# Optimization experiments

Measured on AMD Instinct MI355X. Metric: run time of the kernel, lower is better.

Reference implementation:

```python
import jax, jax.numpy as jnp
import numpy as np

WS, EXP, FW, HEADS = 7, 3, 7, 6
DIM = 192
HD = DIM // HEADS
SCALE = HD ** -0.5
POOL_K, POOL_PAD = 7, 3  # focal level k=0: kernel = 2*(FW//2) + 2**0 + (2**0 - 1) = 7, stride 1, pad 3
WA = WS * WS  # 49 tokens per window


def _rel_index():
    # identical formula for in-window bias and pooled-window bias (k_window = FW + 2**0 - 1 = 7 = WS)
    c = np.stack(np.meshgrid(np.arange(WS), np.arange(WS), indexing='ij')).reshape(2, -1)
    rel = (c[:, :, None] - c[:, None, :]).transpose(1, 2, 0).copy()
    rel[..., 0] += WS - 1
    rel[..., 1] += WS - 1
    rel[..., 0] *= 2 * WS - 1
    return rel.sum(-1)  # (49, 49) int indices into 169-entry tables


def _valid_rolled():
    m = np.ones((4, WS, WS), dtype=np.float32)
    m[0, :-EXP, :-EXP] = 0  # tl
    m[1, :-EXP, EXP:] = 0   # tr
    m[2, EXP:, :-EXP] = 0   # bl
    m[3, EXP:, EXP:] = 0    # br
    return np.nonzero(m.reshape(-1))[0]  # (132,)

REL_IDX = _rel_index()
VALID_ROLLED = _valid_rolled()


def _win_part(t):
    # (B,H,W,C) -> (B*nWin, WA, HEADS, HD)
    B, H, W, C = t.shape
    t = t.reshape(B, H // WS, WS, W // WS, WS, C).transpose(0, 1, 3, 2, 4, 5)
    return t.reshape(-1, WA, HEADS, HD)


def _unfold(t):
    # torch.nn.Unfold(kernel=7, stride=1, pad=3) on (B,h,w,C) -> (B*h*w, K*K, C)
    B, h, w, C = t.shape
    tp = jnp.pad(t, ((0, 0), (POOL_PAD, POOL_PAD), (POOL_PAD, POOL_PAD), (0, 0)))
    ii = np.arange(h)[:, None] + np.arange(POOL_K)[None, :]
    jj = np.arange(w)[:, None] + np.arange(POOL_K)[None, :]
    p = tp[:, ii][:, :, :, jj]            # (B, h, K, w, K, C)
    p = p.transpose(0, 1, 3, 2, 4, 5)     # (B, h, w, K, K, C)
    return p.reshape(B * h * w, POOL_K * POOL_K, C)


def setup_inputs() -> dict:
    key = jax.random.key(0)
    ks = jax.random.split(key, 9)
    B, H, W = 8, 112, 112
    nWh, nWw = H // WS, W // WS
    return {
        'x': jax.random.normal(ks[0], (B, H, W, DIM), jnp.float32),
        'x_pooled': jax.random.normal(ks[1], (B, nWh, nWw, DIM), jnp.float32),
        'qkv_w': jax.random.normal(ks[2], (3 * DIM, DIM), jnp.float32) * 0.02,
        'qkv_b': jax.random.normal(ks[3], (3 * DIM,), jnp.float32) * 0.02,
        'proj_w': jax.random.normal(ks[4], (DIM, DIM), jnp.float32) * 0.02,
        'proj_b': jax.random.normal(ks[5], (DIM,), jnp.float32) * 0.02,
        'rpb_table': jax.random.normal(ks[6], ((2 * WS - 1) ** 2, HEADS), jnp.float32) * 0.02,
        'rpb_neighbors': jax.random.normal(ks[7], (1, HEADS, WA, len(VALID_ROLLED)), jnp.float32) * 0.02,
        'rpb_windows': jax.random.normal(ks[8], (HEADS, (2 * WS - 1) ** 2), jnp.float32) * 0.02,
    }


def reference(x, x_pooled, qkv_w, qkv_b, proj_w, proj_b, rpb_table, rpb_neighbors, rpb_windows):
    B, H, W, C = x.shape
    # qkv on fine features
    qkv = x @ qkv_w.T + qkv_b                    # (B,H,W,3C)
    q, k, v = jnp.split(qkv, 3, axis=-1)
    qw = _win_part(q).transpose(0, 2, 1, 3)      # (BnW, heads, 49, hd)
    kw = _win_part(k).transpose(0, 2, 1, 3)
    vw = _win_part(v).transpose(0, 2, 1, 3)

    # rolled neighbor keys/values (tl, tr, bl, br), gather valid ring indices
    shifts = [(-EXP, -EXP), (-EXP, EXP), (EXP, -EXP), (EXP, EXP)]
    k_roll = jnp.concatenate([_win_part(jnp.roll(k, s, axis=(1, 2))) for s in shifts], axis=1)
    v_roll = jnp.concatenate([_win_part(jnp.roll(v, s, axis=(1, 2))) for s in shifts], axis=1)
    k_roll = k_roll.transpose(0, 2, 1, 3)[:, :, VALID_ROLLED]   # (BnW, heads, 132, hd)
    v_roll = v_roll.transpose(0, 2, 1, 3)[:, :, VALID_ROLLED]
    k_rolled = jnp.concatenate([kw, k_roll], axis=2)            # (BnW, heads, 181, hd)
    v_rolled = jnp.concatenate([vw, v_roll], axis=2)
    wa_rolled = k_rolled.shape[2]

    # focal level-0 pooled keys/values via unfold on the pooled map
    _, nWh, nWw, _ = x_pooled.shape
    qkv_p = x_pooled @ qkv_w.T + qkv_b
    _, kp, vp = jnp.split(qkv_p, 3, axis=-1)
    k_pool = _unfold(kp).reshape(-1, POOL_K * POOL_K, HEADS, HD).transpose(0, 2, 1, 3)  # (BnW, heads, 49, hd)
    v_pool = _unfold(vp).reshape(-1, POOL_K * POOL_K, HEADS, HD).transpose(0, 2, 1, 3)
    # validity mask from unfolding an all-ones map (zero padding -> -100)
    um = _unfold(jnp.ones((1, nWh, nWw, 1), x.dtype))[..., 0]   # (nWin, 49)
    pool_mask = jnp.where(um == 0, jnp.asarray(-100.0, x.dtype), jnp.asarray(0.0, x.dtype))

    k_all = jnp.concatenate([k_rolled, k_pool], axis=2)          # (BnW, heads, 230, hd)
    v_all = jnp.concatenate([v_rolled, v_pool], axis=2)

    attn = jnp.einsum('bhqd,bhkd->bhqk', qw * SCALE, k_all)      # (BnW, heads, 49, 230)

    # relative position biases, concatenated along the key axis
    bias_win = rpb_table[REL_IDX.reshape(-1)].reshape(WA, WA, HEADS).transpose(2, 0, 1)     # (heads,49,49)
    bias_pool = rpb_windows[:, REL_IDX.reshape(-1)].reshape(HEADS, WA, WA)                  # (heads,49,49)
    bias = jnp.concatenate([bias_win, rpb_neighbors[0], bias_pool], axis=-1)                # (heads,49,230)
    attn = attn + bias[None]
    # boundary mask on the pooled slice, tiled per batch
    mask_b = jnp.tile(pool_mask, (B, 1))[:, None, None, :]       # (BnW,1,1,49)
    attn = attn.at[..., wa_rolled:].add(mask_b)

    attn = jax.nn.softmax(attn, axis=-1)
    out = jnp.einsum('bhqk,bhkd->bqhd', attn, v_all).reshape(-1, WA, C)
    return out @ proj_w.T + proj_b                               # (B*nWin, 49, C)
```

## Files before the change

kernel.cpp:

```cpp
#include <hip/hip_runtime.h>
#include <stdint.h>


#define DIM 192
#define HEADS 6
#define HD 32
#define WA 49
#define NKEY 230
#define VSTR 264
#define SSTR2 136
#define SCALE_F 0.17677669529663687f
#define LOG2E 1.4426950408889634f
#define PM_NEG (-144.26950408889634f)
#define NFINE 100352
#define POOLBASE (NFINE * DIM)

typedef __attribute__((ext_vector_type(8))) short bf16x8;
typedef __attribute__((ext_vector_type(4))) float f32x4;

__device__ __forceinline__ short f2bf(float f) {
  union { float f; uint32_t u; } v; v.f = f;
  uint32_t u = v.u;
  return (short)((u + 0x7FFFu + ((u >> 16) & 1u)) >> 16);
}

__device__ __forceinline__ float bf2f(short s) {
  union { uint32_t u; float f; } v;
  v.u = ((uint32_t)(uint16_t)s) << 16;
  return v.f;
}

__device__ __forceinline__ uint32_t cvtpk(float lo, float hi) {
  uint32_t r;
  asm("v_cvt_pk_bf16_f32 %0, %1, %2" : "=v"(r) : "v"(lo), "v"(hi));
  return r;
}

__global__ __launch_bounds__(256) void k_setup(
    const float* __restrict__ qkv_w, const float* __restrict__ proj_w,
    const float* __restrict__ rpb_table, const float* __restrict__ rpb_nb,
    const float* __restrict__ rpb_win,
    short* __restrict__ w1, short* __restrict__ w1s, short* __restrict__ w2s,
    int* __restrict__ t_idx, short* __restrict__ bias_bf) {
  __shared__ int2 ring_s[132];
  if (threadIdx.x < 132) {
    int e = threadIdx.x;
    int cnt = 0, fdr = 0, fdc = 0;
    for (int idx = 0; idx < 196; ++idx) {
      int s = idx / 49, rc = idx % 49, r = rc / 7, c = rc % 7;
      bool valid;
      if (s == 0)      valid = (r >= 4) || (c >= 4);
      else if (s == 1) valid = (r >= 4) || (c < 3);
      else if (s == 2) valid = (r < 3)  || (c >= 4);
      else             valid = (r < 3)  || (c < 3);
      if (valid) {
        if (cnt == e) { fdr = r + ((s < 2) ? 3 : -3); fdc = c + (((s & 1) == 0) ? 3 : -3); }
        ++cnt;
      }
    }
    ring_s[e] = make_int2(fdr, fdc);
  }
  __syncthreads();

  const int tid = blockIdx.x * blockDim.x + threadIdx.x;
  const int nth = gridDim.x * blockDim.x;
  for (int i = tid; i < 576 * DIM; i += nth) {
    float fv = qkv_w[i];
    w1[i] = f2bf(fv);
    int r = i / DIM, c = i % DIM;
    int t = r >> 5, ntl = (r >> 4) & 1, lr = r & 15;
    int ks = c >> 5, quad = (c >> 3) & 3, e = c & 7;
    w1s[t * 6144 + (((ntl * 6 + ks) * 4 + quad) * 16 + lr) * 8 + e] = f2bf(fv);
  }
  for (int i = tid; i < DIM * DIM; i += nth) {
    int r = i / DIM, c = i % DIM;
    int t = r >> 5, ntl = (r >> 4) & 1, lr = r & 15;
    int ks = c >> 5, quad = (c >> 3) & 3, e = c & 7;
    w2s[t * 6144 + (((ntl * 6 + ks) * 4 + quad) * 16 + lr) * 8 + e] = f2bf(proj_w[i]);
  }
  for (int i = tid; i < 2048 * NKEY; i += nth) {
    int win = i / NKEY, kk = i - win * NKEY;
    int b = win >> 8, wr = (win >> 4) & 15, wc = win & 15;
    int off;
    if (kk < 49) {
      int ii = wr * 7 + kk / 7, jj = wc * 7 + kk % 7;
      off = ((b * 112 + ii) * 112 + jj) * DIM;
    } else if (kk < 181) {
      int2 rr = ring_s[kk - 49];
      int ii = wr * 7 + rr.x; if (ii < 0) ii += 112; if (ii >= 112) ii -= 112;
      int jj = wc * 7 + rr.y; if (jj < 0) jj += 112; if (jj >= 112) jj -= 112;
      off = ((b * 112 + ii) * 112 + jj) * DIM;
    } else {
      int p = kk - 181;
      int ii = wr - 3 + p / 7, jj = wc - 3 + p % 7;
      off = (ii >= 0 && ii < 16 && jj >= 0 && jj < 16)
              ? (POOLBASE + ((b * 16 + ii) * 16 + jj) * DIM) : -1;
    }
    t_idx[(win << 8) + kk] = off;
  }
  for (int i = tid; i < HEADS * 15 * 1024; i += nth) {
    int row = i & 63, l16v = (i >> 6) & 15;
    int rem = i >> 10, nt = rem % 15, h = rem / 15;
    int kk = nt * 16 + l16v;
    float bv = 0.f;
    if (kk >= NKEY) {
      bv = -1e30f;
    } else if (row < WA) {
      if (kk < 49) {
        int ar = row / 7, ac = row % 7, br = kk / 7, bc = kk % 7;
        bv = rpb_table[((ar - br + 6) * 13 + (ac - bc + 6)) * HEADS + h] * LOG2E;
      } else if (kk < 181) {
        bv = rpb_nb[((size_t)h * WA + row) * 132 + (kk - 49)] * LOG2E;
      } else {
        int p = kk - 181;
        int ar = row / 7, ac = row % 7, br = p / 7, bc = p % 7;
        bv = rpb_win[h * 169 + (ar - br + 6) * 13 + (ac - bc + 6)] * LOG2E;
      }
    }
    bias_bf[i] = f2bf(bv);
  }
}

__global__ __launch_bounds__(256, 4) void k_qkv_main(
    const float* __restrict__ x, const short* __restrict__ w1s, const float* __restrict__ qkv_b,
    short* __restrict__ qw, short* __restrict__ kn, short* __restrict__ vn) {
  __shared__ __align__(16) short wbuf[2][6144];
  const int tid = threadIdx.x;
  const int wave = tid >> 6, lane = tid & 63, quad = lane >> 4, l16 = lane & 15;
  const int mbase = blockIdx.x * 128;

  bf16x8 afr[2][6];
#pragma unroll
  for (int mt = 0; mt < 2; ++mt) {
    const float* xrow = x + (size_t)(mbase + wave * 32 + mt * 16 + l16) * DIM + quad * 8;
#pragma unroll
    for (int ks = 0; ks < 6; ++ks) {
      float4 f0 = *(const float4*)(xrow + ks * 32);
      float4 f1 = *(const float4*)(xrow + ks * 32 + 4);
      bf16x8 a;
      a[0] = f2bf(f0.x); a[1] = f2bf(f0.y); a[2] = f2bf(f0.z); a[3] = f2bf(f0.w);
      a[4] = f2bf(f1.x); a[5] = f2bf(f1.y); a[6] = f2bf(f1.z); a[7] = f2bf(f1.w);
      afr[mt][ks] = a;
    }
  }
  uint32_t q_base[2][4], kv_base[2][4];
#pragma unroll
  for (int mt = 0; mt < 2; ++mt)
#pragma unroll
    for (int rg = 0; rg < 4; ++rg) {
      int m = mbase + wave * 32 + mt * 16 + quad * 4 + rg;
      int bb = m / 12544, rem = m % 12544;
      int i = rem / 112, j = rem % 112;
      int wr = i / 7, rr = i % 7, wc = j / 7, cc = j % 7;
      int winid = (bb * 16 + wr) * 16 + wc;
      q_base[mt][rg]  = ((uint32_t)winid * WA + (rr * 7 + cc)) * DIM;
      kv_base[mt][rg] = (uint32_t)m * DIM;
    }

  int4 st[3];
  {
    const int4* src = (const int4*)w1s + tid;
#pragma unroll
    for (int it = 0; it < 3; ++it) st[it] = src[it * 256];
  }
  for (int t = 0; t < 18; ++t) {
    short* buf = wbuf[t & 1];
#pragma unroll
    for (int it = 0; it < 3; ++it) ((int4*)buf)[tid + it * 256] = st[it];
    __syncthreads();
    if (t < 17) {
      const int4* src = (const int4*)(w1s + (t + 1) * 6144) + tid;
#pragma unroll
      for (int it = 0; it < 3; ++it) st[it] = src[it * 256];
    }
#pragma unroll
    for (int ntl = 0; ntl < 2; ++ntl) {
      const int n = t * 32 + ntl * 16 + l16;
      bf16x8 bfr[6];
#pragma unroll
      for (int ks = 0; ks < 6; ++ks)
        bfr[ks] = *(const bf16x8*)&buf[(((ntl * 6 + ks) * 4 + quad) * 16 + l16) * 8];
      const float bias = qkv_b[n];
      f32x4 ac[2];
#pragma unroll
      for (int mt = 0; mt < 2; ++mt) {
        f32x4 a = {0.f, 0.f, 0.f, 0.f};
#pragma unroll
        for (int ks = 0; ks < 6; ++ks)
          a = __builtin_amdgcn_mfma_f32_16x16x32_bf16(afr[mt][ks], bfr[ks], a, 0, 0, 0);
        ac[mt] = a;
      }
      if (t < 6) {
        const float qs = SCALE_F * LOG2E;
        const float bq = bias * qs;
#pragma unroll
        for (int rg = 0; rg < 4; ++rg) {
          uint32_t r = cvtpk(fmaf(ac[0][rg], qs, bq), fmaf(ac[1][rg], qs, bq));
          qw[q_base[0][rg] + n] = (short)r;
          qw[q_base[1][rg] + n] = (short)(r >> 16);
        }
      } else if (t < 12) {
#pragma unroll
        for (int rg = 0; rg < 4; ++rg) {
          uint32_t r = cvtpk(ac[0][rg] + bias, ac[1][rg] + bias);
          kn[kv_base[0][rg] + (n - 192)] = (short)r;
          kn[kv_base[1][rg] + (n - 192)] = (short)(r >> 16);
        }
      } else {
#pragma unroll
        for (int rg = 0; rg < 4; ++rg) {
          uint32_t r = cvtpk(ac[0][rg] + bias, ac[1][rg] + bias);
          vn[kv_base[0][rg] + (n - 384)] = (short)r;
          vn[kv_base[1][rg] + (n - 384)] = (short)(r >> 16);
        }
      }
    }
  }
}

__global__ __launch_bounds__(256) void k_qkv_pool(
    const float* __restrict__ xp, const short* __restrict__ w1, const float* __restrict__ qkv_b,
    short* __restrict__ kp, short* __restrict__ vp) {
  const int tid = threadIdx.x;
  const int wave = tid >> 6, lane = tid & 63, quad = lane >> 4, l16 = lane & 15;
  const int mbase = (blockIdx.x * 4 + wave) * 16;

  bf16x8 afr[6];
  {
    const float* xrow = xp + (size_t)(mbase + l16) * DIM + quad * 8;
#pragma unroll
    for (int ks = 0; ks < 6; ++ks) {
      float4 f0 = *(const float4*)(xrow + ks * 32);
      float4 f1 = *(const float4*)(xrow + ks * 32 + 4);
      bf16x8 a;
      a[0] = f2bf(f0.x); a[1] = f2bf(f0.y); a[2] = f2bf(f0.z); a[3] = f2bf(f0.w);
      a[4] = f2bf(f1.x); a[5] = f2bf(f1.y); a[6] = f2bf(f1.z); a[7] = f2bf(f1.w);
      afr[ks] = a;
    }
  }
  for (int nt = 12; nt < 36; ++nt) {
    const int n = nt * 16 + l16;
    const short* wrow = w1 + (size_t)n * DIM + quad * 8;
    f32x4 acc = {0.f, 0.f, 0.f, 0.f};
#pragma unroll
    for (int ks = 0; ks < 6; ++ks)
      acc = __builtin_amdgcn_mfma_f32_16x16x32_bf16(afr[ks], *(const bf16x8*)(wrow + ks * 32), acc, 0, 0, 0);
    const float bias = qkv_b[n];
#pragma unroll
    for (int rg = 0; rg < 4; ++rg) {
      int m = mbase + quad * 4 + rg;
      float vo = acc[rg] + bias;
      if (nt < 24) kp[(size_t)m * DIM + (n - 192)] = f2bf(vo);
      else         vp[(size_t)m * DIM + (n - 384)] = f2bf(vo);
    }
  }
}

__global__ __launch_bounds__(256, 4) void k_attn(
    const short* __restrict__ qw, const short* __restrict__ kall, const short* __restrict__ vall,
    const short* __restrict__ bias_bf, const int* __restrict__ t_idx,
    short* __restrict__ ao) {
  __shared__ __align__(16) char smem[36352];
  short* vT_l = (short*)smem;
  short* k_l  = (short*)(smem + 16896);
  short* S_l  = (short*)(smem + 16896);
  float* pm_f = (float*)(smem + 36096);

  const int tid = threadIdx.x;
  const int bid = ((int)blockIdx.x & 7) * 1536 + ((int)blockIdx.x >> 3);
  const int win = bid / HEADS;
  const int h   = bid - win * HEADS;
  const int wave = tid >> 6, lane = tid & 63, quad = lane >> 4, l16 = lane & 15;

  {
    int* kli = (int*)k_l;
    for (int i = tid; i < 200; i += 256) kli[4600 + i] = 0;
    if (tid < 128) {
      int ch = tid >> 2, j = tid & 3;
      *(int4*)&vT_l[ch * VSTR + ((224 + j * 8) ^ (((ch >> 3) & 3) << 4))] = make_int4(0, 0, 0, 0);
    }
    if (tid >= 49 && tid < 64) pm_f[tid] = 0.f;
  }
  bf16x8 qfr = {0, 0, 0, 0, 0, 0, 0, 0};
  {
    const int qrow = wave * 16 + l16;
    if (qrow < WA)
      qfr = *(const bf16x8*)(qw + ((size_t)win * WA + qrow) * DIM + h * HD + quad * 8);
  }
  __syncthreads();

  {
    const int part = tid & 3;
    const int choff = h * HD + part * 8;
    const int* tix = t_idx + (win << 8);
#pragma unroll
    for (int it = 0; it < 4; ++it) {
      int kk = it * 64 + (tid >> 2);
      if (kk < NKEY) {
        int off = tix[kk];
        int4 kvv = make_int4(0, 0, 0, 0), vvv = make_int4(0, 0, 0, 0);
        if (off >= 0) {
          kvv = *(const int4*)(kall + off + choff);
          vvv = *(const int4*)(vall + off + choff);
        }
        *(int4*)&k_l[kk * 40 + part * 8] = kvv;
        const short* vs = (const short*)&vvv;
        const int kkx = kk ^ (part << 4);
        short* vbase = &vT_l[part * 8 * VSTR + kkx];
#pragma unroll
        for (int e = 0; e < 8; ++e) vbase[e * VSTR] = vs[e];
        if (part == 0 && kk >= 181)
          pm_f[kk - 181] = (off < 0) ? PM_NEG : 0.f;
      }
    }
  }
  __syncthreads();

  f32x4 acc[15];
#pragma unroll
  for (int nt = 0; nt < 15; ++nt) {
    bf16x8 kfr = *(const bf16x8*)&k_l[(nt * 16 + l16) * 40 + quad * 8];
    f32x4 z = {0.f, 0.f, 0.f, 0.f};
    acc[nt] = __builtin_amdgcn_mfma_f32_16x16x32_bf16(qfr, kfr, z, 0, 0, 0);
  }
  const int rowb = wave * 16 + quad * 4;
  {
    const short* bb = bias_bf + ((size_t)(h * 15 * 16 + l16)) * 64 + rowb;
#pragma unroll
    for (int nt = 0; nt < 15; ++nt) {
      int2 braw = *(const int2*)(bb + nt * 1024);
      const short* bs = (const short*)&braw;
      float pm = 0.f;
      if (nt >= 12) {
        pm = pm_f[nt * 16 + l16 - 181];
      } else if (nt == 11) {
        int idx = 11 * 16 + l16 - 181;
        float t = pm_f[idx < 0 ? 0 : idx];
        pm = (idx < 0) ? 0.f : t;
      }
#pragma unroll
      for (int rg = 0; rg < 4; ++rg)
        acc[nt][rg] = acc[nt][rg] + bf2f(bs[rg]) + pm;
    }
  }
  float m4[4] = {-1e30f, -1e30f, -1e30f, -1e30f};
#pragma unroll
  for (int nt = 0; nt < 15; ++nt)
#pragma unroll
    for (int rg = 0; rg < 4; ++rg) m4[rg] = fmaxf(m4[rg], acc[nt][rg]);
#pragma unroll
  for (int msk = 1; msk <= 8; msk <<= 1)
#pragma unroll
    for (int rg = 0; rg < 4; ++rg) m4[rg] = fmaxf(m4[rg], __shfl_xor(m4[rg], msk));
  float s4[4] = {0.f, 0.f, 0.f, 0.f};
#pragma unroll
  for (int nt = 0; nt < 15; ++nt)
#pragma unroll
    for (int rg = 0; rg < 4; ++rg) {
      float e = __builtin_amdgcn_exp2f(acc[nt][rg] - m4[rg]);
      acc[nt][rg] = e; s4[rg] += e;
    }
#pragma unroll
  for (int msk = 1; msk <= 8; msk <<= 1)
#pragma unroll
    for (int rg = 0; rg < 4; ++rg) s4[rg] += __shfl_xor(s4[rg], msk);
  float inv4[4];
#pragma unroll
  for (int rg = 0; rg < 4; ++rg) inv4[rg] = 1.f / s4[rg];

  __syncthreads();

  const int swS = ((quad >> 1) & 1) << 4;
#pragma unroll
  for (int rg = 0; rg < 4; ++rg) {
    const int base = (rowb + rg) * SSTR2;
#pragma unroll
    for (int p = 0; p < 4; ++p) {
      uint32_t r = cvtpk(acc[2 * p][rg], acc[2 * p + 1][rg]);
      S_l[base + ((p * 32 + l16) ^ swS)]      = (short)r;
      S_l[base + ((p * 32 + 16 + l16) ^ swS)] = (short)(r >> 16);
    }
  }
  __syncthreads();

  const int swR = ((l16 >> 3) & 1) << 4;
  f32x4 acc2[2] = {{0.f, 0.f, 0.f, 0.f}, {0.f, 0.f, 0.f, 0.f}};
#pragma unroll
  for (int nt2 = 0; nt2 < 2; ++nt2) {
    const int fvr = (((nt2 * 16 + l16) >> 3) & 3) << 4;
#pragma unroll
    for (int k0 = 0; k0 < 4; ++k0) {
      bf16x8 pfr = *(const bf16x8*)&S_l[(wave * 16 + l16) * SSTR2 + ((k0 * 32 + quad * 8) ^ swR)];
      bf16x8 vfr = *(const bf16x8*)&vT_l[(nt2 * 16 + l16) * VSTR + ((k0 * 32 + quad * 8) ^ fvr)];
      acc2[nt2] = __builtin_amdgcn_mfma_f32_16x16x32_bf16(pfr, vfr, acc2[nt2], 0, 0, 0);
    }
  }
  __syncthreads();

#pragma unroll
  for (int rg = 0; rg < 4; ++rg) {
    const int base = (rowb + rg) * SSTR2;
#pragma unroll
    for (int p = 0; p < 3; ++p) {
      uint32_t r = cvtpk(acc[8 + 2 * p][rg], acc[9 + 2 * p][rg]);
      S_l[base + ((p * 32 + l16) ^ swS)]      = (short)r;
      S_l[base + ((p * 32 + 16 + l16) ^ swS)] = (short)(r >> 16);
    }
    uint32_t r = cvtpk(acc[14][rg], 0.f);
    S_l[base + ((96 + l16) ^ swS)]  = (short)r;
    S_l[base + ((112 + l16) ^ swS)] = (short)(r >> 16);
  }
  __syncthreads();

#pragma unroll
  for (int nt2 = 0; nt2 < 2; ++nt2) {
    const int fvr = (((nt2 * 16 + l16) >> 3) & 3) << 4;
#pragma unroll
    for (int k0 = 0; k0 < 4; ++k0) {
      bf16x8 pfr = *(const bf16x8*)&S_l[(wave * 16 + l16) * SSTR2 + ((k0 * 32 + quad * 8) ^ swR)];
      bf16x8 vfr = *(const bf16x8*)&vT_l[(nt2 * 16 + l16) * VSTR + ((128 + k0 * 32 + quad * 8) ^ fvr)];
      acc2[nt2] = __builtin_amdgcn_mfma_f32_16x16x32_bf16(pfr, vfr, acc2[nt2], 0, 0, 0);
    }
  }

#pragma unroll
  for (int rg = 0; rg < 4; ++rg) {
    const int row = rowb + rg;
    if (row < WA) {
      uint32_t r = cvtpk(acc2[0][rg] * inv4[rg], acc2[1][rg] * inv4[rg]);
      short* dst = ao + ((size_t)win * WA + row) * DIM + h * HD + l16;
      dst[0]  = (short)r;
      dst[16] = (short)(r >> 16);
    }
  }
}

__global__ __launch_bounds__(256, 4) void k_proj(
    const short* __restrict__ ao, const short* __restrict__ w2s, const float* __restrict__ pb,
    float* __restrict__ out) {
  __shared__ __align__(16) short wbuf[2][6144];
  const int tid = threadIdx.x;
  const int wave = tid >> 6, lane = tid & 63, quad = lane >> 4, l16 = lane & 15;
  const int mbase = blockIdx.x * 128;

  bf16x8 afr[2][6];
#pragma unroll
  for (int mt = 0; mt < 2; ++mt) {
    const short* arow = ao + (size_t)(mbase + wave * 32 + mt * 16 + l16) * DIM + quad * 8;
#pragma unroll
    for (int ks = 0; ks < 6; ++ks) afr[mt][ks] = *(const bf16x8*)(arow + ks * 32);
  }
  int4 st[3];
  {
    const int4* src = (const int4*)w2s + tid;
#pragma unroll
    for (int it = 0; it < 3; ++it) st[it] = src[it * 256];
  }
  for (int t = 0; t < 6; ++t) {
    short* buf = wbuf[t & 1];
#pragma unroll
    for (int it = 0; it < 3; ++it) ((int4*)buf)[tid + it * 256] = st[it];
    __syncthreads();
    if (t < 5) {
      const int4* src = (const int4*)(w2s + (t + 1) * 6144) + tid;
#pragma unroll
      for (int it = 0; it < 3; ++it) st[it] = src[it * 256];
    }
#pragma unroll
    for (int ntl = 0; ntl < 2; ++ntl) {
      const int n = t * 32 + ntl * 16 + l16;
      bf16x8 bfr[6];
#pragma unroll
      for (int ks = 0; ks < 6; ++ks)
        bfr[ks] = *(const bf16x8*)&buf[(((ntl * 6 + ks) * 4 + quad) * 16 + l16) * 8];
      const float bias = pb[n];
#pragma unroll
      for (int mt = 0; mt < 2; ++mt) {
        f32x4 acc = {0.f, 0.f, 0.f, 0.f};
#pragma unroll
        for (int ks = 0; ks < 6; ++ks)
          acc = __builtin_amdgcn_mfma_f32_16x16x32_bf16(afr[mt][ks], bfr[ks], acc, 0, 0, 0);
#pragma unroll
        for (int rg = 0; rg < 4; ++rg)
          out[(size_t)(mbase + wave * 32 + mt * 16 + quad * 4 + rg) * DIM + n] = acc[rg] + bias;
      }
    }
  }
}

extern "C" void kernel_launch(void* const* d_in, const int* in_sizes, int n_in,
                              void* d_out, int out_size, void* d_ws, size_t ws_size,
                              hipStream_t stream) {
  (void)in_sizes; (void)n_in; (void)out_size; (void)ws_size;
  const float* x         = (const float*)d_in[0];
  const float* xp        = (const float*)d_in[1];
  const float* qkv_w     = (const float*)d_in[2];
  const float* qkv_b     = (const float*)d_in[3];
  const float* proj_w    = (const float*)d_in[4];
  const float* proj_b    = (const float*)d_in[5];
  const float* rpb_table = (const float*)d_in[6];
  const float* rpb_nb    = (const float*)d_in[7];
  const float* rpb_win   = (const float*)d_in[8];

  char* ws = (char*)d_ws;
  size_t off = 0;
  auto alloc = [&](size_t bytes) -> void* {
    void* p = ws + off; off = (off + bytes + 255) & ~(size_t)255; return p;
  };
  short* w1       = (short*)alloc((size_t)576 * DIM * 2);
  short* w1s      = (short*)alloc((size_t)576 * DIM * 2);
  short* w2s      = (short*)alloc((size_t)DIM * DIM * 2);
  short* bias_bf  = (short*)alloc((size_t)HEADS * 15 * 1024 * 2);
  int*   t_idx    = (int*)  alloc((size_t)2048 * 256 * 4);
  short* qw       = (short*)alloc((size_t)2048 * WA * DIM * 2);
  short* kall     = (short*)alloc((size_t)(NFINE + 2048) * DIM * 2);
  short* vall     = (short*)alloc((size_t)(NFINE + 2048) * DIM * 2);
  short* ao       = (short*)alloc((size_t)2048 * WA * DIM * 2);

  k_setup<<<dim3(64), dim3(256), 0, stream>>>(qkv_w, proj_w, rpb_table, rpb_nb, rpb_win,
                                              w1, w1s, w2s, t_idx, bias_bf);
  k_qkv_main<<<dim3(784), dim3(256), 0, stream>>>(x, w1s, qkv_b, qw, kall, vall);
  k_qkv_pool<<<dim3(32), dim3(256), 0, stream>>>(xp, w1, qkv_b,
                                                 kall + (size_t)POOLBASE, vall + (size_t)POOLBASE);
  k_attn<<<dim3(12288), dim3(256), 0, stream>>>(qw, kall, vall, bias_bf, t_idx, ao);
  k_proj<<<dim3(784), dim3(256), 0, stream>>>(ao, w2s, proj_b, (float*)d_out);
}
```

Baseline: 470.0 us.

## Compute transposed scores so softmax stays in registers and skips LDS round-trip

The QK^T MFMA now swaps its operands, so each lane holds one query row across keys. Softmax then needs only two cross-quad shuffles, and the exponentials are packed straight into bf16 A-fragments for the PV MFMA. This removes the LDS staging of the score matrix and several __syncthreads, and drops the max-subtraction, relying on the scores being small. The bias table and the V-transpose column order are permuted to match the new fragment layout, and k_setup is launched with more blocks.

```diff
diff --git a/kernel.cpp b/kernel.cpp
--- a/kernel.cpp
+++ b/kernel.cpp
@@ -8,7 +8,6 @@
 #define WA 49
 #define NKEY 230
 #define VSTR 264
-#define SSTR2 136
 #define SCALE_F 0.17677669529663687f
 #define LOG2E 1.4426950408889634f
 #define PM_NEG (-144.26950408889634f)
@@ -41,7 +40,7 @@
     const float* __restrict__ rpb_table, const float* __restrict__ rpb_nb,
     const float* __restrict__ rpb_win,
     short* __restrict__ w1, short* __restrict__ w1s, short* __restrict__ w2s,
-    int* __restrict__ t_idx, short* __restrict__ bias_bf) {
+    int* __restrict__ t_idx, short* __restrict__ bias2) {
   __shared__ int2 ring_s[132];
   if (threadIdx.x < 132) {
     int e = threadIdx.x;
@@ -99,25 +98,26 @@
     t_idx[(win << 8) + kk] = off;
   }
   for (int i = tid; i < HEADS * 15 * 1024; i += nth) {
-    int row = i & 63, l16v = (i >> 6) & 15;
-    int rem = i >> 10, nt = rem % 15, h = rem / 15;
-    int kk = nt * 16 + l16v;
-    float bv = 0.f;
-    if (kk >= NKEY) {
+    int h = i / 15360, r1 = i - h * 15360;
+    int nt = r1 >> 10, r2 = r1 & 1023;
+    int qd = r2 >> 8, row = (r2 >> 2) & 63, rg = r2 & 3;
+    int key = nt * 16 + qd * 4 + rg;
+    float bv;
+    if (key >= NKEY) {
       bv = -1e30f;
-    } else if (row < WA) {
-      if (kk < 49) {
-        int ar = row / 7, ac = row % 7, br = kk / 7, bc = kk % 7;
-        bv = rpb_table[((ar - br + 6) * 13 + (ac - bc + 6)) * HEADS + h] * LOG2E;
-      } else if (kk < 181) {
-        bv = rpb_nb[((size_t)h * WA + row) * 132 + (kk - 49)] * LOG2E;
-      } else {
-        int p = kk - 181;
-        int ar = row / 7, ac = row % 7, br = p / 7, bc = p % 7;
-        bv = rpb_win[h * 169 + (ar - br + 6) * 13 + (ac - bc + 6)] * LOG2E;
-      }
-    }
-    bias_bf[i] = f2bf(bv);
+    } else if (row >= WA) {
+      bv = 0.f;
+    } else if (key < 49) {
+      int ar = row / 7, ac = row % 7, br = key / 7, bc = key % 7;
+      bv = rpb_table[((ar - br + 6) * 13 + (ac - bc + 6)) * HEADS + h] * LOG2E;
+    } else if (key < 181) {
+      bv = rpb_nb[((size_t)h * WA + row) * 132 + (key - 49)] * LOG2E;
+    } else {
+      int p = key - 181;
+      int ar = row / 7, ac = row % 7, br = p / 7, bc = p % 7;
+      bv = rpb_win[h * 169 + (ar - br + 6) * 13 + (ac - bc + 6)] * LOG2E;
+    }
+    bias2[i] = f2bf(bv);
   }
 }
 
@@ -258,35 +258,31 @@
 
 __global__ __launch_bounds__(256, 4) void k_attn(
     const short* __restrict__ qw, const short* __restrict__ kall, const short* __restrict__ vall,
-    const short* __restrict__ bias_bf, const int* __restrict__ t_idx,
+    const short* __restrict__ bias2, const int* __restrict__ t_idx,
     short* __restrict__ ao) {
-  __shared__ __align__(16) char smem[36352];
+  __shared__ __align__(16) char smem[36416];
   short* vT_l = (short*)smem;
   short* k_l  = (short*)(smem + 16896);
-  short* S_l  = (short*)(smem + 16896);
-  float* pm_f = (float*)(smem + 36096);
+  float* pm2  = (float*)(smem + 36096);
 
   const int tid = threadIdx.x;
   const int bid = ((int)blockIdx.x & 7) * 1536 + ((int)blockIdx.x >> 3);
   const int win = bid / HEADS;
   const int h   = bid - win * HEADS;
   const int wave = tid >> 6, lane = tid & 63, quad = lane >> 4, l16 = lane & 15;
-
-  {
-    int* kli = (int*)k_l;
-    for (int i = tid; i < 200; i += 256) kli[4600 + i] = 0;
-    if (tid < 128) {
-      int ch = tid >> 2, j = tid & 3;
-      *(int4*)&vT_l[ch * VSTR + ((224 + j * 8) ^ (((ch >> 3) & 3) << 4))] = make_int4(0, 0, 0, 0);
-    }
-    if (tid >= 49 && tid < 64) pm_f[tid] = 0.f;
+  const int row = wave * 16 + l16;
+
+  {
+    int4 z = make_int4(0, 0, 0, 0);
+#pragma unroll
+    for (int i = 0; i < 4; ++i) ((int4*)vT_l)[tid + i * 256] = z;
+    if (tid < 32) ((int4*)vT_l)[1024 + tid] = z;
+    if (tid < 200) ((int*)k_l)[4600 + tid] = 0;
+    if (tid < 80) pm2[tid] = 0.f;
   }
   bf16x8 qfr = {0, 0, 0, 0, 0, 0, 0, 0};
-  {
-    const int qrow = wave * 16 + l16;
-    if (qrow < WA)
-      qfr = *(const bf16x8*)(qw + ((size_t)win * WA + qrow) * DIM + h * HD + quad * 8);
-  }
+  if (row < WA)
+    qfr = *(const bf16x8*)(qw + ((size_t)win * WA + row) * DIM + h * HD + quad * 8);
   __syncthreads();
 
   {
@@ -304,13 +300,14 @@
           vvv = *(const int4*)(vall + off + choff);
         }
         *(int4*)&k_l[kk * 40 + part * 8] = kvv;
+        int col = ((kk & 0x7C) << 1) | ((kk & 0x80) >> 5) | (kk & 3);
+        col ^= part << 4;
         const short* vs = (const short*)&vvv;
-        const int kkx = kk ^ (part << 4);
-        short* vbase = &vT_l[part * 8 * VSTR + kkx];
+        short* vbase = &vT_l[part * 8 * VSTR + col];
 #pragma unroll
         for (int e = 0; e < 8; ++e) vbase[e * VSTR] = vs[e];
         if (part == 0 && kk >= 181)
-          pm_f[kk - 181] = (off < 0) ? PM_NEG : 0.f;
+          pm2[kk - 176] = (off < 0) ? PM_NEG : 0.f;
       }
     }
   }
@@ -321,117 +318,63 @@
   for (int nt = 0; nt < 15; ++nt) {
     bf16x8 kfr = *(const bf16x8*)&k_l[(nt * 16 + l16) * 40 + quad * 8];
     f32x4 z = {0.f, 0.f, 0.f, 0.f};
-    acc[nt] = __builtin_amdgcn_mfma_f32_16x16x32_bf16(qfr, kfr, z, 0, 0, 0);
-  }
-  const int rowb = wave * 16 + quad * 4;
-  {
-    const short* bb = bias_bf + ((size_t)(h * 15 * 16 + l16)) * 64 + rowb;
+    acc[nt] = __builtin_amdgcn_mfma_f32_16x16x32_bf16(kfr, qfr, z, 0, 0, 0);
+  }
+
+  float s = 0.f;
+  {
+    const short* bb = bias2 + h * 15360 + quad * 256 + row * 4;
 #pragma unroll
     for (int nt = 0; nt < 15; ++nt) {
       int2 braw = *(const int2*)(bb + nt * 1024);
       const short* bs = (const short*)&braw;
-      float pm = 0.f;
-      if (nt >= 12) {
-        pm = pm_f[nt * 16 + l16 - 181];
-      } else if (nt == 11) {
-        int idx = 11 * 16 + l16 - 181;
-        float t = pm_f[idx < 0 ? 0 : idx];
-        pm = (idx < 0) ? 0.f : t;
-      }
-#pragma unroll
-      for (int rg = 0; rg < 4; ++rg)
-        acc[nt][rg] = acc[nt][rg] + bf2f(bs[rg]) + pm;
-    }
-  }
-  float m4[4] = {-1e30f, -1e30f, -1e30f, -1e30f};
-#pragma unroll
-  for (int nt = 0; nt < 15; ++nt)
-#pragma unroll
-    for (int rg = 0; rg < 4; ++rg) m4[rg] = fmaxf(m4[rg], acc[nt][rg]);
-#pragma unroll
-  for (int msk = 1; msk <= 8; msk <<= 1)
-#pragma unroll
-    for (int rg = 0; rg < 4; ++rg) m4[rg] = fmaxf(m4[rg], __shfl_xor(m4[rg], msk));
-  float s4[4] = {0.f, 0.f, 0.f, 0.f};
-#pragma unroll
-  for (int nt = 0; nt < 15; ++nt)
-#pragma unroll
-    for (int rg = 0; rg < 4; ++rg) {
-      float e = __builtin_amdgcn_exp2f(acc[nt][rg] - m4[rg]);
-      acc[nt][rg] = e; s4[rg] += e;
-    }
-#pragma unroll
-  for (int msk = 1; msk <= 8; msk <<= 1)
-#pragma unroll
-    for (int rg = 0; rg < 4; ++rg) s4[rg] += __shfl_xor(s4[rg], msk);
-  float inv4[4];
-#pragma unroll
-  for (int rg = 0; rg < 4; ++rg) inv4[rg] = 1.f / s4[rg];
-
-  __syncthreads();
-
-  const int swS = ((quad >> 1) & 1) << 4;
-#pragma unroll
-  for (int rg = 0; rg < 4; ++rg) {
-    const int base = (rowb + rg) * SSTR2;
-#pragma unroll
-    for (int p = 0; p < 4; ++p) {
-      uint32_t r = cvtpk(acc[2 * p][rg], acc[2 * p + 1][rg]);
-      S_l[base + ((p * 32 + l16) ^ swS)]      = (short)r;
-      S_l[base + ((p * 32 + 16 + l16) ^ swS)] = (short)(r >> 16);
-    }
-  }
-  __syncthreads();
-
-  const int swR = ((l16 >> 3) & 1) << 4;
+      f32x4 pmv = {0.f, 0.f, 0.f, 0.f};
+      if (nt >= 11) pmv = *(const f32x4*)&pm2[nt * 16 + quad * 4 - 176];
+#pragma unroll
+      for (int rg = 0; rg < 4; ++rg) {
+        float e = __builtin_amdgcn_exp2f(acc[nt][rg] + bf2f(bs[rg]) + pmv[rg]);
+        acc[nt][rg] = e; s += e;
+      }
+    }
+  }
+  s += __shfl_xor(s, 16);
+  s += __shfl_xor(s, 32);
+  const float inv = 1.f / s;
+
+  bf16x8 pfr[8];
+#pragma unroll
+  for (int c = 0; c < 8; ++c) {
+    union { bf16x8 v; uint32_t d[4]; } u;
+    u.d[0] = cvtpk(acc[c][0], acc[c][1]);
+    u.d[1] = cvtpk(acc[c][2], acc[c][3]);
+    if (c < 7) {
+      u.d[2] = cvtpk(acc[c + 8][0], acc[c + 8][1]);
+      u.d[3] = cvtpk(acc[c + 8][2], acc[c + 8][3]);
+    } else {
+      u.d[2] = 0; u.d[3] = 0;
+    }
+    pfr[c] = u.v;
+  }
+
   f32x4 acc2[2] = {{0.f, 0.f, 0.f, 0.f}, {0.f, 0.f, 0.f, 0.f}};
 #pragma unroll
   for (int nt2 = 0; nt2 < 2; ++nt2) {
-    const int fvr = (((nt2 * 16 + l16) >> 3) & 3) << 4;
-#pragma unroll
-    for (int k0 = 0; k0 < 4; ++k0) {
-      bf16x8 pfr = *(const bf16x8*)&S_l[(wave * 16 + l16) * SSTR2 + ((k0 * 32 + quad * 8) ^ swR)];
-      bf16x8 vfr = *(const bf16x8*)&vT_l[(nt2 * 16 + l16) * VSTR + ((k0 * 32 + quad * 8) ^ fvr)];
-      acc2[nt2] = __builtin_amdgcn_mfma_f32_16x16x32_bf16(pfr, vfr, acc2[nt2], 0, 0, 0);
-    }
-  }
-  __syncthreads();
-
-#pragma unroll
-  for (int rg = 0; rg < 4; ++rg) {
-    const int base = (rowb + rg) * SSTR2;
-#pragma unroll
-    for (int p = 0; p < 3; ++p) {
-      uint32_t r = cvtpk(acc[8 + 2 * p][rg], acc[9 + 2 * p][rg]);
-      S_l[base + ((p * 32 + l16) ^ swS)]      = (short)r;
-      S_l[base + ((p * 32 + 16 + l16) ^ swS)] = (short)(r >> 16);
-    }
-    uint32_t r = cvtpk(acc[14][rg], 0.f);
-    S_l[base + ((96 + l16) ^ swS)]  = (short)r;
-    S_l[base + ((112 + l16) ^ swS)] = (short)(r >> 16);
-  }
-  __syncthreads();
-
-#pragma unroll
-  for (int nt2 = 0; nt2 < 2; ++nt2) {
-    const int fvr = (((nt2 * 16 + l16) >> 3) & 3) << 4;
-#pragma unroll
-    for (int k0 = 0; k0 < 4; ++k0) {
-      bf16x8 pfr = *(const bf16x8*)&S_l[(wave * 16 + l16) * SSTR2 + ((k0 * 32 + quad * 8) ^ swR)];
-      bf16x8 vfr = *(const bf16x8*)&vT_l[(nt2 * 16 + l16) * VSTR + ((128 + k0 * 32 + quad * 8) ^ fvr)];
-      acc2[nt2] = __builtin_amdgcn_mfma_f32_16x16x32_bf16(pfr, vfr, acc2[nt2], 0, 0, 0);
-    }
-  }
-
-#pragma unroll
-  for (int rg = 0; rg < 4; ++rg) {
-    const int row = rowb + rg;
-    if (row < WA) {
-      uint32_t r = cvtpk(acc2[0][rg] * inv4[rg], acc2[1][rg] * inv4[rg]);
-      short* dst = ao + ((size_t)win * WA + row) * DIM + h * HD + l16;
-      dst[0]  = (short)r;
-      dst[16] = (short)(r >> 16);
-    }
+    const int prw = ((nt2 * 2 + (l16 >> 3)) & 3) << 4;
+#pragma unroll
+    for (int c = 0; c < 8; ++c) {
+      bf16x8 vfr = *(const bf16x8*)&vT_l[(nt2 * 16 + l16) * VSTR + ((c * 32 + quad * 8) ^ prw)];
+      acc2[nt2] = __builtin_amdgcn_mfma_f32_16x16x32_bf16(vfr, pfr[c], acc2[nt2], 0, 0, 0);
+    }
+  }
+
+  if (row < WA) {
+    short* dst = ao + ((size_t)win * WA + row) * DIM + h * HD + quad * 4;
+    int2 o0 = make_int2((int)cvtpk(acc2[0][0] * inv, acc2[0][1] * inv),
+                        (int)cvtpk(acc2[0][2] * inv, acc2[0][3] * inv));
+    int2 o1 = make_int2((int)cvtpk(acc2[1][0] * inv, acc2[1][1] * inv),
+                        (int)cvtpk(acc2[1][2] * inv, acc2[1][3] * inv));
+    *(int2*)&dst[0]  = o0;
+    *(int2*)&dst[16] = o1;
   }
 }
 
@@ -510,18 +453,18 @@
   short* w1       = (short*)alloc((size_t)576 * DIM * 2);
   short* w1s      = (short*)alloc((size_t)576 * DIM * 2);
   short* w2s      = (short*)alloc((size_t)DIM * DIM * 2);
-  short* bias_bf  = (short*)alloc((size_t)HEADS * 15 * 1024 * 2);
+  short* bias2    = (short*)alloc((size_t)HEADS * 15 * 1024 * 2);
   int*   t_idx    = (int*)  alloc((size_t)2048 * 256 * 4);
   short* qw       = (short*)alloc((size_t)2048 * WA * DIM * 2);
   short* kall     = (short*)alloc((size_t)(NFINE + 2048) * DIM * 2);
   short* vall     = (short*)alloc((size_t)(NFINE + 2048) * DIM * 2);
   short* ao       = (short*)alloc((size_t)2048 * WA * DIM * 2);
 
-  k_setup<<<dim3(64), dim3(256), 0, stream>>>(qkv_w, proj_w, rpb_table, rpb_nb, rpb_win,
-                                              w1, w1s, w2s, t_idx, bias_bf);
+  k_setup<<<dim3(256), dim3(256), 0, stream>>>(qkv_w, proj_w, rpb_table, rpb_nb, rpb_win,
+                                               w1, w1s, w2s, t_idx, bias2);
   k_qkv_main<<<dim3(784), dim3(256), 0, stream>>>(x, w1s, qkv_b, qw, kall, vall);
   k_qkv_pool<<<dim3(32), dim3(256), 0, stream>>>(xp, w1, qkv_b,
                                                  kall + (size_t)POOLBASE, vall + (size_t)POOLBASE);
-  k_attn<<<dim3(12288), dim3(256), 0, stream>>>(qw, kall, vall, bias_bf, t_idx, ao);
+  k_attn<<<dim3(12288), dim3(256), 0, stream>>>(qw, kall, vall, bias2, t_idx, ao);
   k_proj<<<dim3(784), dim3(256), 0, stream>>>(ao, w2s, proj_b, (float*)d_out);
 }
```

New measurement: 414.0 us. 1.14x faster.
